# Optimization experiments

Hardware: AMD Instinct MI355X
Metric: run time of the kernel (lower is better)

The kernel has to match this reference:

```python
import jax, jax.numpy as jnp
import numpy as np

TEMPERATURE = 0.07
B = 4096   # simclr batch
D = 256    # projection dim
N = 8192   # num cells for spatial loss
P = 4096   # num spatial positive pairs


def setup_inputs() -> dict:
    key = jax.random.key(0)
    k1, k2, k3, k4, k5 = jax.random.split(key, 5)
    z1 = jax.random.normal(k1, (B, D), dtype=jnp.float32)
    z2 = jax.random.normal(k2, (B, D), dtype=jnp.float32)
    embeddings = jax.random.normal(k3, (N, D), dtype=jnp.float32)
    anchor_idx = jax.random.randint(k4, (P,), 0, N)
    neighbor_idx = jax.random.randint(k5, (P,), 0, N)
    return {"z1": z1, "z2": z2, "embeddings": embeddings,
            "anchor_idx": anchor_idx, "neighbor_idx": neighbor_idx}


def _l2norm(x, eps=1e-12):
    return x / jnp.maximum(jnp.linalg.norm(x, axis=1, keepdims=True), eps)


def _simclr_loss(z1, z2, temperature):
    b = z1.shape[0]
    z = jnp.concatenate([_l2norm(z1), _l2norm(z2)], axis=0)      # [2B, D]
    sim = (z @ z.T) / temperature                                 # [2B, 2B]
    exp_sim = jnp.exp(sim)
    n2 = 2 * b
    # sum over all columns excluding the diagonal (as in the torch code)
    sum_exp = jnp.sum(exp_sim, axis=1) - jnp.diagonal(exp_sim)
    # positive pair index: i <-> i+b
    pair = jnp.concatenate([jnp.arange(b) + b, jnp.arange(b)])
    pos_exp = exp_sim[jnp.arange(n2), pair]
    return jnp.mean(-jnp.log(pos_exp / sum_exp))


def _spatial_contrastive_loss(embeddings, anchor_idx, neighbor_idx, temperature):
    e = _l2norm(embeddings)                                       # [N, D]
    a = e[anchor_idx]                                             # [P, D]
    nb = e[neighbor_idx]                                          # [P, D]
    pos = jnp.sum(a * nb, axis=1) / temperature                   # [P]
    sims = (a @ e.T) / temperature                                # [P, N]
    cols = jnp.arange(e.shape[0])[None, :]
    neg_mask = (cols == anchor_idx[:, None]) | (cols == neighbor_idx[:, None])
    sims = jnp.where(neg_mask, -jnp.inf, sims)
    # cross entropy with the positive at label 0: -pos + logsumexp([pos, negs])
    logits = jnp.concatenate([pos[:, None], sims], axis=1)        # [P, 1+N]
    lse = jax.nn.logsumexp(logits, axis=1)
    return jnp.mean(lse - pos)


def reference(z1, z2, embeddings, anchor_idx, neighbor_idx):
    l_simclr = _simclr_loss(z1, z2, TEMPERATURE)
    l_spatial = _spatial_contrastive_loss(embeddings, anchor_idx, neighbor_idx, TEMPERATURE)
    return jnp.stack([l_simclr, l_spatial])   # [2]
```

## Files before the change

kernel.cpp:

```cpp
#include <hip/hip_runtime.h>
#include <stdint.h>

#define NB 4096
#define ND 256
#define NN 8192
#define NP 4096

#define K_SIGMA 4.5398156f
#define LN2F    0.6931471805599453f

typedef __attribute__((ext_vector_type(8))) short short8;
typedef __attribute__((ext_vector_type(4))) float f32x4;

__device__ __forceinline__ float bf2f(uint16_t u) {
  union { uint32_t i; float f; } v; v.i = ((uint32_t)u) << 16; return v.f;
}
__device__ __forceinline__ uint16_t f2bf(float f) {
  union { float f; uint32_t i; } v; v.f = f;
  uint32_t b = v.i;
  b += 0x7FFF + ((b >> 16) & 1);
  return (uint16_t)(b >> 16);
}

__global__ __launch_bounds__(256) void normalize_kernel(
    const float* __restrict__ z1, const float* __restrict__ z2,
    const float* __restrict__ emb,
    uint16_t* __restrict__ zb, uint16_t* __restrict__ eb)
{
  const int w = threadIdx.x >> 6, lane = threadIdx.x & 63;
  const int row = blockIdx.x * 4 + w;
  const float* src;
  uint16_t* dst;
  if (row < 4096)      { src = z1  + row * 256;          dst = zb + row * 256; }
  else if (row < 8192) { src = z2  + (row - 4096) * 256; dst = zb + row * 256; }
  else                 { src = emb + (row - 8192) * 256; dst = eb + (row - 8192) * 256; }
  float4 v = *reinterpret_cast<const float4*>(src + lane * 4);
  float ss = v.x * v.x + v.y * v.y + v.z * v.z + v.w * v.w;
#pragma unroll
  for (int m = 1; m < 64; m <<= 1) ss += __shfl_xor(ss, m);
  float inv = K_SIGMA / fmaxf(sqrtf(ss), 1e-12f);
  ushort4 o;
  o.x = f2bf(v.x * inv); o.y = f2bf(v.y * inv);
  o.z = f2bf(v.z * inv); o.w = f2bf(v.w * inv);
  *reinterpret_cast<ushort4*>(dst + lane * 4) = o;
}

__global__ __launch_bounds__(256) void sweep_kernel(
    const uint16_t* __restrict__ zb, const uint16_t* __restrict__ eb,
    const int* __restrict__ anchor,
    float* __restrict__ rs_z, float* __restrict__ rs_s)
{
  __shared__ __align__(16) uint16_t lds[64 * 256];
  const int bid  = blockIdx.x;
  const int tid  = threadIdx.x;
  const int w    = tid >> 6;
  const int lane = tid & 63;

  const bool spatial = (bid >= 512);
  const int sub = spatial ? (bid - 512) : bid;
  const int rb  = sub >> 3;
  const int cc  = sub & 7;
  const uint16_t* __restrict__ Amat = spatial ? eb : zb;
  const uint16_t* __restrict__ Bmat = spatial ? eb : zb;
  float* __restrict__ rs = spatial ? rs_s : rs_z;

  const int row_base = rb * 128 + w * 32;

  short8 afrag[2][8];
#pragma unroll
  for (int t = 0; t < 2; ++t) {
    int r  = row_base + t * 16 + (lane & 15);
    int sr = spatial ? anchor[r] : r;
    const uint16_t* ap = Amat + sr * 256 + ((lane >> 4) * 8);
#pragma unroll
    for (int ks = 0; ks < 8; ++ks)
      afrag[t][ks] = *reinterpret_cast<const short8*>(ap + ks * 32);
  }

  float rsacc[2][4];
#pragma unroll
  for (int t = 0; t < 2; ++t)
#pragma unroll
    for (int r = 0; r < 4; ++r) rsacc[t][r] = 0.0f;

  const int cbase = cc * 1024;
  const int r_ = tid >> 5;
  const int c_ = tid & 31;
  const int src_chunk = c_ ^ r_;

  for (int step = 0; step < 16; ++step) {
    const int col0 = cbase + step * 64;
    __syncthreads();
#pragma unroll
    for (int it = 0; it < 8; ++it) {
      const uint16_t* src = Bmat + (col0 + it * 8 + r_) * 256 + src_chunk * 8;
      uint16_t* dst = &lds[(it * 8 + r_) * 256 + c_ * 8];
      __builtin_amdgcn_global_load_lds(
          (const __attribute__((address_space(1))) void*)src,
          (__attribute__((address_space(3))) void*)dst, 16, 0, 0);
    }
    __syncthreads();

    f32x4 acc[2][4];
#pragma unroll
    for (int t = 0; t < 2; ++t)
#pragma unroll
      for (int ct = 0; ct < 4; ++ct) {
        f32x4 z = {0.0f, 0.0f, 0.0f, 0.0f};
        acc[t][ct] = z;
      }

#pragma unroll
    for (int ks = 0; ks < 8; ++ks) {
#pragma unroll
      for (int ct = 0; ct < 4; ++ct) {
        const int brow = ct * 16 + (lane & 15);
        const int ch   = (ks * 4 + (lane >> 4)) ^ (brow & 7);
        short8 bfrag = *reinterpret_cast<const short8*>(&lds[(brow * 32 + ch) * 8]);
        acc[0][ct] = __builtin_amdgcn_mfma_f32_16x16x32_bf16(afrag[0][ks], bfrag, acc[0][ct], 0, 0, 0);
        acc[1][ct] = __builtin_amdgcn_mfma_f32_16x16x32_bf16(afrag[1][ks], bfrag, acc[1][ct], 0, 0, 0);
      }
    }

#pragma unroll
    for (int t = 0; t < 2; ++t)
#pragma unroll
      for (int ct = 0; ct < 4; ++ct)
#pragma unroll
        for (int r = 0; r < 4; ++r)
          rsacc[t][r] += exp2f(acc[t][ct][r]);
  }

#pragma unroll
  for (int t = 0; t < 2; ++t)
#pragma unroll
    for (int r = 0; r < 4; ++r) {
      float v = rsacc[t][r];
      v += __shfl_xor(v, 1);
      v += __shfl_xor(v, 2);
      v += __shfl_xor(v, 4);
      v += __shfl_xor(v, 8);
      if ((lane & 15) == 0) {
        int row = row_base + t * 16 + (lane >> 4) * 4 + r;
        atomicAdd(&rs[row], v);
      }
    }
}

__global__ __launch_bounds__(256) void finalize_kernel(
    const uint16_t* __restrict__ zb, const uint16_t* __restrict__ eb,
    const int* __restrict__ anchor, const int* __restrict__ neighbor,
    const float* __restrict__ rs_z, const float* __restrict__ rs_s,
    float* __restrict__ loss_z, float* __restrict__ loss_s)
{
  const int w = threadIdx.x >> 6, lane = threadIdx.x & 63;
  const int row = blockIdx.x * 4 + w;
  const uint16_t *pa, *pb;
  const bool is_z = (row < 8192);
  int idx;
  bool same = false;
  if (is_z) {
    idx = row;
    int pair = (row < 4096) ? row + 4096 : row - 4096;
    pa = zb + row * 256;
    pb = zb + pair * 256;
  } else {
    idx = row - 8192;
    int ai = anchor[idx], ni = neighbor[idx];
    same = (ai == ni);
    pa = eb + ai * 256;
    pb = eb + ni * 256;
  }
  ushort4 ua = *reinterpret_cast<const ushort4*>(pa + lane * 4);
  ushort4 ub = *reinterpret_cast<const ushort4*>(pb + lane * 4);
  float a0 = bf2f(ua.x), a1 = bf2f(ua.y), a2 = bf2f(ua.z), a3 = bf2f(ua.w);
  float b0 = bf2f(ub.x), b1 = bf2f(ub.y), b2 = bf2f(ub.z), b3 = bf2f(ub.w);
  float dd = a0 * a0 + a1 * a1 + a2 * a2 + a3 * a3;
  float dn = a0 * b0 + a1 * b1 + a2 * b2 + a3 * b3;
#pragma unroll
  for (int m = 1; m < 64; m <<= 1) {
    dd += __shfl_xor(dd, m);
    dn += __shfl_xor(dn, m);
  }
  if (lane == 0) {
    if (is_z) {
      loss_z[idx] = logf(rs_z[idx] - exp2f(dd)) - dn * LN2F;
    } else {
      float S = rs_s[idx] - exp2f(dd) + (same ? exp2f(dn) : 0.0f);
      loss_s[idx] = logf(S) - dn * LN2F;
    }
  }
}

__global__ __launch_bounds__(256) void reduce_kernel(
    const float* __restrict__ loss_z, const float* __restrict__ loss_s,
    float* __restrict__ out)
{
  const int which = blockIdx.x;
  const float* src = which ? loss_s : loss_z;
  const int n = which ? 4096 : 8192;
  float s = 0.0f;
  for (int i = threadIdx.x; i < n; i += 256) s += src[i];
#pragma unroll
  for (int m = 1; m < 64; m <<= 1) s += __shfl_xor(s, m);
  __shared__ float ps[4];
  if ((threadIdx.x & 63) == 0) ps[threadIdx.x >> 6] = s;
  __syncthreads();
  if (threadIdx.x == 0)
    out[which] = (ps[0] + ps[1] + ps[2] + ps[3]) * (which ? (1.0f / 4096.0f) : (1.0f / 8192.0f));
}

extern "C" void kernel_launch(void* const* d_in, const int* in_sizes, int n_in,
                              void* d_out, int out_size, void* d_ws, size_t ws_size,
                              hipStream_t stream) {
  const float* z1      = (const float*)d_in[0];
  const float* z2      = (const float*)d_in[1];
  const float* emb     = (const float*)d_in[2];
  const int*   anchor  = (const int*)d_in[3];
  const int*   neighbor= (const int*)d_in[4];
  float* out = (float*)d_out;

  float* ws      = (float*)d_ws;
  float* rs_z    = ws;
  float* rs_s    = ws + 8192;
  float* loss_z  = ws + 12288;
  float* loss_s  = ws + 20480;
  uint16_t* zb   = (uint16_t*)(ws + 24576);
  uint16_t* eb   = zb + 8192 * 256;

  hipMemsetAsync(ws, 0, 12288 * sizeof(float), stream);
  normalize_kernel<<<4096, 256, 0, stream>>>(z1, z2, emb, zb, eb);
  sweep_kernel<<<768, 256, 0, stream>>>(zb, eb, anchor, rs_z, rs_s);
  finalize_kernel<<<3072, 256, 0, stream>>>(zb, eb, anchor, neighbor,
                                            rs_z, rs_s, loss_z, loss_s);
  reduce_kernel<<<2, 256, 0, stream>>>(loss_z, loss_s, out);
}
```

Baseline: 152.1 us.

## Switch sweep to 32x32 MFMA tiles with double-buffered LDS and fold memset

```diff
diff --git a/kernel.cpp b/kernel.cpp
--- a/kernel.cpp
+++ b/kernel.cpp
@@ -1,16 +1,11 @@
 #include <hip/hip_runtime.h>
 #include <stdint.h>
 
-#define NB 4096
-#define ND 256
-#define NN 8192
-#define NP 4096
-
 #define K_SIGMA 4.5398156f
 #define LN2F    0.6931471805599453f
 
-typedef __attribute__((ext_vector_type(8))) short short8;
-typedef __attribute__((ext_vector_type(4))) float f32x4;
+typedef __attribute__((ext_vector_type(8)))  short short8;
+typedef __attribute__((ext_vector_type(16))) float f32x16;
 
 __device__ __forceinline__ float bf2f(uint16_t u) {
   union { uint32_t i; float f; } v; v.i = ((uint32_t)u) << 16; return v.f;
@@ -25,8 +20,12 @@
 __global__ __launch_bounds__(256) void normalize_kernel(
     const float* __restrict__ z1, const float* __restrict__ z2,
     const float* __restrict__ emb,
-    uint16_t* __restrict__ zb, uint16_t* __restrict__ eb)
-{
+    uint16_t* __restrict__ zb, uint16_t* __restrict__ eb,
+    float* __restrict__ rs0)
+{
+  const int gtid = blockIdx.x * 256 + threadIdx.x;
+  if (gtid < 12288) rs0[gtid] = 0.0f;
+
   const int w = threadIdx.x >> 6, lane = threadIdx.x & 63;
   const int row = blockIdx.x * 4 + w;
   const float* src;
@@ -45,103 +44,112 @@
   *reinterpret_cast<ushort4*>(dst + lane * 4) = o;
 }
 
-__global__ __launch_bounds__(256) void sweep_kernel(
+__global__ __launch_bounds__(256, 2) void sweep_kernel(
     const uint16_t* __restrict__ zb, const uint16_t* __restrict__ eb,
     const int* __restrict__ anchor,
     float* __restrict__ rs_z, float* __restrict__ rs_s)
 {
-  __shared__ __align__(16) uint16_t lds[64 * 256];
+  __shared__ __align__(16) uint16_t lds[2][64 * 256];
   const int bid  = blockIdx.x;
   const int tid  = threadIdx.x;
   const int w    = tid >> 6;
   const int lane = tid & 63;
 
-  const bool spatial = (bid >= 512);
-  const int sub = spatial ? (bid - 512) : bid;
-  const int rb  = sub >> 3;
-  const int cc  = sub & 7;
+  const bool spatial = (bid >= 1024);
+  const int sub = spatial ? (bid - 1024) : bid;
+  const int rb  = sub >> 5;
+  const int cc  = sub & 31;
   const uint16_t* __restrict__ Amat = spatial ? eb : zb;
   const uint16_t* __restrict__ Bmat = spatial ? eb : zb;
   float* __restrict__ rs = spatial ? rs_s : rs_z;
 
-  const int row_base = rb * 128 + w * 32;
-
-  short8 afrag[2][8];
+  const int row_base = rb * 256 + w * 64;
+  const int hi = lane >> 5;
+  const int ln = lane & 31;
+
+  short8 afrag[2][16];
 #pragma unroll
   for (int t = 0; t < 2; ++t) {
-    int r  = row_base + t * 16 + (lane & 15);
+    int r  = row_base + t * 32 + ln;
     int sr = spatial ? anchor[r] : r;
-    const uint16_t* ap = Amat + sr * 256 + ((lane >> 4) * 8);
-#pragma unroll
-    for (int ks = 0; ks < 8; ++ks)
-      afrag[t][ks] = *reinterpret_cast<const short8*>(ap + ks * 32);
-  }
-
-  float rsacc[2][4];
+    const uint16_t* ap = Amat + sr * 256 + hi * 8;
+#pragma unroll
+    for (int ks = 0; ks < 16; ++ks)
+      afrag[t][ks] = *reinterpret_cast<const short8*>(ap + ks * 16);
+  }
+
+  float rsacc[2][16];
 #pragma unroll
   for (int t = 0; t < 2; ++t)
 #pragma unroll
-    for (int r = 0; r < 4; ++r) rsacc[t][r] = 0.0f;
-
-  const int cbase = cc * 1024;
+    for (int r = 0; r < 16; ++r) rsacc[t][r] = 0.0f;
+
+  const int cbase = cc * 256;
   const int r_ = tid >> 5;
   const int c_ = tid & 31;
   const int src_chunk = c_ ^ r_;
 
-  for (int step = 0; step < 16; ++step) {
+  auto STAGE = [&](int buf, int step) {
     const int col0 = cbase + step * 64;
-    __syncthreads();
 #pragma unroll
     for (int it = 0; it < 8; ++it) {
       const uint16_t* src = Bmat + (col0 + it * 8 + r_) * 256 + src_chunk * 8;
-      uint16_t* dst = &lds[(it * 8 + r_) * 256 + c_ * 8];
+      uint16_t* dst = &lds[buf][(it * 8 + r_) * 256 + c_ * 8];
       __builtin_amdgcn_global_load_lds(
           (const __attribute__((address_space(1))) void*)src,
           (__attribute__((address_space(3))) void*)dst, 16, 0, 0);
     }
+  };
+
+  STAGE(0, 0);
+  __syncthreads();
+  int cur = 0;
+
+  for (int step = 0; step < 4; ++step) {
+    if (step < 3) STAGE(cur ^ 1, step + 1);
+
+    f32x16 acc[2][2];
+#pragma unroll
+    for (int t = 0; t < 2; ++t)
+#pragma unroll
+      for (int ct = 0; ct < 2; ++ct)
+#pragma unroll
+        for (int r = 0; r < 16; ++r) acc[t][ct][r] = 0.0f;
+
+#pragma unroll
+    for (int ks = 0; ks < 16; ++ks) {
+#pragma unroll
+      for (int ct = 0; ct < 2; ++ct) {
+        const int brow = ct * 32 + ln;
+        const int ch   = (ks * 2 + hi) ^ (brow & 7);
+        short8 bfrag = *reinterpret_cast<const short8*>(&lds[cur][brow * 256 + ch * 8]);
+        acc[0][ct] = __builtin_amdgcn_mfma_f32_32x32x16_bf16(afrag[0][ks], bfrag, acc[0][ct], 0, 0, 0);
+        acc[1][ct] = __builtin_amdgcn_mfma_f32_32x32x16_bf16(afrag[1][ks], bfrag, acc[1][ct], 0, 0, 0);
+      }
+    }
+
+#pragma unroll
+    for (int t = 0; t < 2; ++t)
+#pragma unroll
+      for (int r = 0; r < 16; ++r)
+        rsacc[t][r] += exp2f(acc[t][0][r]) + exp2f(acc[t][1][r]);
+
     __syncthreads();
-
-    f32x4 acc[2][4];
-#pragma unroll
-    for (int t = 0; t < 2; ++t)
-#pragma unroll
-      for (int ct = 0; ct < 4; ++ct) {
-        f32x4 z = {0.0f, 0.0f, 0.0f, 0.0f};
-        acc[t][ct] = z;
-      }
-
-#pragma unroll
-    for (int ks = 0; ks < 8; ++ks) {
-#pragma unroll
-      for (int ct = 0; ct < 4; ++ct) {
-        const int brow = ct * 16 + (lane & 15);
-        const int ch   = (ks * 4 + (lane >> 4)) ^ (brow & 7);
-        short8 bfrag = *reinterpret_cast<const short8*>(&lds[(brow * 32 + ch) * 8]);
-        acc[0][ct] = __builtin_amdgcn_mfma_f32_16x16x32_bf16(afrag[0][ks], bfrag, acc[0][ct], 0, 0, 0);
-        acc[1][ct] = __builtin_amdgcn_mfma_f32_16x16x32_bf16(afrag[1][ks], bfrag, acc[1][ct], 0, 0, 0);
-      }
-    }
-
-#pragma unroll
-    for (int t = 0; t < 2; ++t)
-#pragma unroll
-      for (int ct = 0; ct < 4; ++ct)
-#pragma unroll
-        for (int r = 0; r < 4; ++r)
-          rsacc[t][r] += exp2f(acc[t][ct][r]);
+    cur ^= 1;
   }
 
 #pragma unroll
   for (int t = 0; t < 2; ++t)
 #pragma unroll
-    for (int r = 0; r < 4; ++r) {
+    for (int r = 0; r < 16; ++r) {
       float v = rsacc[t][r];
       v += __shfl_xor(v, 1);
       v += __shfl_xor(v, 2);
       v += __shfl_xor(v, 4);
       v += __shfl_xor(v, 8);
-      if ((lane & 15) == 0) {
-        int row = row_base + t * 16 + (lane >> 4) * 4 + r;
+      v += __shfl_xor(v, 16);
+      if (ln == 0) {
+        int row = row_base + t * 32 + (r & 3) + 8 * (r >> 2) + 4 * hi;
         atomicAdd(&rs[row], v);
       }
     }
@@ -228,9 +236,8 @@
   uint16_t* zb   = (uint16_t*)(ws + 24576);
   uint16_t* eb   = zb + 8192 * 256;
 
-  hipMemsetAsync(ws, 0, 12288 * sizeof(float), stream);
-  normalize_kernel<<<4096, 256, 0, stream>>>(z1, z2, emb, zb, eb);
-  sweep_kernel<<<768, 256, 0, stream>>>(zb, eb, anchor, rs_z, rs_s);
+  normalize_kernel<<<4096, 256, 0, stream>>>(z1, z2, emb, zb, eb, ws);
+  sweep_kernel<<<1536, 256, 0, stream>>>(zb, eb, anchor, rs_z, rs_s);
   finalize_kernel<<<3072, 256, 0, stream>>>(zb, eb, anchor, neighbor,
                                             rs_z, rs_s, loss_z, loss_s);
   reduce_kernel<<<2, 256, 0, stream>>>(loss_z, loss_s, out);
```

Measured after the change: 334.4 us. 2.2x slower.
